# Performance work log

Measured on AMD Instinct MI355X. Metric: run time of the kernel, lower is better.

## Reference

```python
import jax, jax.numpy as jnp
import numpy as np

B, T, D = 4, 4096, 1024
EPS = 1e-5


def _layernorm(x, w):
    mu = jnp.mean(x, axis=-1, keepdims=True)
    var = jnp.var(x, axis=-1, keepdims=True)
    return (x - mu) * jax.lax.rsqrt(var + EPS) * w


def setup_inputs() -> dict:
    key = jax.random.key(0)
    k0, k1, k2, k3 = jax.random.split(key, 4)
    x = jax.random.normal(k0, (B, T, D), dtype=jnp.float32)
    lengths = jax.random.randint(k1, (B,), 1, T + 1, dtype=jnp.int32)
    ln1_w = jnp.ones((D,), dtype=jnp.float32)
    ln2_w = jnp.ones((D,), dtype=jnp.float32)
    Wfc = jax.random.normal(k2, (D, 4 * D), dtype=jnp.float32) * 0.02
    Wproj = jax.random.normal(k3, (4 * D, D), dtype=jnp.float32) * 0.02
    return {"x": x, "lengths": lengths, "ln1_w": ln1_w, "ln2_w": ln2_w,
            "Wfc": Wfc, "Wproj": Wproj}


def reference(x, lengths, ln1_w, ln2_w, Wfc, Wproj):
    b, t, d = x.shape
    # valid[b, i] = i < lengths[b]  (non-padded positions)
    valid = (jnp.arange(t)[None, :] < lengths[:, None]).astype(x.dtype)  # (B,T)

    # --- FusedQueryAtt: out[b,i] = h[b,i] + valid_i * sum_{j<=i} valid_j * gelu(h[b,j])
    h = _layernorm(x, ln1_w)
    g = jax.nn.gelu(h, approximate=False) * valid[:, :, None]  # (B,T,D)
    attn_out = h + valid[:, :, None] * jnp.cumsum(g, axis=1)
    x = x + attn_out  # residual around attn

    # --- MLP (bias=False, dropout=0 in eval)
    h2 = _layernorm(x, ln2_w)
    mlp_out = jax.nn.gelu(h2 @ Wfc, approximate=False) @ Wproj
    return x + mlp_out
```

## Files before the change

### kernel.cpp

```cpp
#include <hip/hip_runtime.h>
#include <hip/hip_bf16.h>
#include <math.h>

#define B_SZ 4
#define T_SZ 4096
#define D_SZ 1024
#define H_SZ 4096
#define CHUNK 16
#define NCHUNK (T_SZ / CHUNK)
#define LN_EPS 1e-5f

using frag8 = __attribute__((ext_vector_type(8))) short;
using f32x4 = __attribute__((ext_vector_type(4))) float;

__device__ __forceinline__ float gelu_exact(float x) {
  return 0.5f * x * (1.0f + erff(x * 0.70710678118654752f));
}

__device__ __forceinline__ float gelu_fast(float x) {
  float u2 = 1.5957691216057308f * (x + 0.044715f * x * x * x);
  float e = __expf(u2);
  return x - x * __builtin_amdgcn_rcpf(e + 1.0f);
}

__device__ __forceinline__ unsigned short f2bf(float f) {
  unsigned u = __float_as_uint(f);
  u += 0x7fffu + ((u >> 16) & 1u);
  return (unsigned short)(u >> 16);
}

__global__ __launch_bounds__(256) void ln_stats(
    const float* __restrict__ x, float2* __restrict__ stats) {
  __shared__ float red[8];
  int tid = threadIdx.x;
  size_t row = (size_t)blockIdx.x * D_SZ;
  float4 v = ((const float4*)(x + row))[tid];
  float s = v.x + v.y + v.z + v.w;
  float q = v.x * v.x + v.y * v.y + v.z * v.z + v.w * v.w;
#pragma unroll
  for (int o = 32; o > 0; o >>= 1) {
    s += __shfl_xor(s, o, 64);
    q += __shfl_xor(q, o, 64);
  }
  int w = tid >> 6;
  if ((tid & 63) == 0) { red[w * 2] = s; red[w * 2 + 1] = q; }
  __syncthreads();
  if (tid == 0) {
    s = red[0] + red[2] + red[4] + red[6];
    q = red[1] + red[3] + red[5] + red[7];
    float mu = s * (1.0f / D_SZ);
    float var = q * (1.0f / D_SZ) - mu * mu;
    float2 st; st.x = mu; st.y = rsqrtf(var + LN_EPS);
    stats[blockIdx.x] = st;
  }
}

__global__ __launch_bounds__(256) void attn_phase1(
    const float* __restrict__ x, const float2* __restrict__ stats,
    const int* __restrict__ lengths, const float* __restrict__ w1,
    float* __restrict__ partial, float* __restrict__ csum) {
  int b = blockIdx.x >> 8;
  int c = blockIdx.x & (NCHUNK - 1);
  int tid = threadIdx.x;
  int len = lengths[b];
  float4 w = ((const float4*)w1)[tid];
  float run0 = 0.f, run1 = 0.f, run2 = 0.f, run3 = 0.f;
#pragma unroll 4
  for (int i = 0; i < CHUNK; ++i) {
    int t = c * CHUNK + i;
    size_t row = ((size_t)b * T_SZ + t) * D_SZ;
    float4 v = ((const float4*)(x + row))[tid];
    float2 st = stats[b * T_SZ + t];
    bool valid = t < len;
    float hx = (v.x - st.x) * st.y * w.x, hy = (v.y - st.x) * st.y * w.y;
    float hz = (v.z - st.x) * st.y * w.z, hw = (v.w - st.x) * st.y * w.w;
    if (valid) {
      run0 += gelu_exact(hx); run1 += gelu_exact(hy);
      run2 += gelu_exact(hz); run3 += gelu_exact(hw);
    }
    float4 p;
    p.x = v.x + hx + (valid ? run0 : 0.f);
    p.y = v.y + hy + (valid ? run1 : 0.f);
    p.z = v.z + hz + (valid ? run2 : 0.f);
    p.w = v.w + hw + (valid ? run3 : 0.f);
    ((float4*)(partial + row))[tid] = p;
  }
  float4 cs; cs.x = run0; cs.y = run1; cs.z = run2; cs.w = run3;
  ((float4*)(csum + ((size_t)b * NCHUNK + c) * D_SZ))[tid] = cs;
}

__global__ __launch_bounds__(256) void chunk_scan(float* __restrict__ csum) {
  int idx = blockIdx.x * 256 + threadIdx.x;
  int b = idx >> 10;
  int d = idx & (D_SZ - 1);
  float* p = csum + (size_t)b * NCHUNK * D_SZ + d;
  float acc = 0.f;
#pragma unroll 8
  for (int c = 0; c < NCHUNK; ++c) {
    float t = p[(size_t)c * D_SZ];
    p[(size_t)c * D_SZ] = acc;
    acc += t;
  }
}

__global__ __launch_bounds__(256) void attn_phase2_ln2(
    float* __restrict__ xres, const float* __restrict__ csum,
    const int* __restrict__ lengths, const float* __restrict__ w2,
    unsigned short* __restrict__ h2) {
  __shared__ float red[8];
  int t = blockIdx.x & (T_SZ - 1);
  int b = blockIdx.x >> 12;
  int tid = threadIdx.x;
  bool valid = t < lengths[b];
  int c = t / CHUNK;
  size_t row = ((size_t)b * T_SZ + t) * D_SZ;
  float4 v = ((const float4*)(xres + row))[tid];
  if (valid) {
    float4 o = ((const float4*)(csum + ((size_t)b * NCHUNK + c) * D_SZ))[tid];
    v.x += o.x; v.y += o.y; v.z += o.z; v.w += o.w;
  }
  ((float4*)(xres + row))[tid] = v;
  float s = v.x + v.y + v.z + v.w;
  float q = v.x * v.x + v.y * v.y + v.z * v.z + v.w * v.w;
#pragma unroll
  for (int o = 32; o > 0; o >>= 1) {
    s += __shfl_xor(s, o, 64);
    q += __shfl_xor(q, o, 64);
  }
  int wv = tid >> 6;
  if ((tid & 63) == 0) { red[wv * 2] = s; red[wv * 2 + 1] = q; }
  __syncthreads();
  s = red[0] + red[2] + red[4] + red[6];
  q = red[1] + red[3] + red[5] + red[7];
  float mu = s * (1.0f / D_SZ);
  float var = q * (1.0f / D_SZ) - mu * mu;
  float rstd = rsqrtf(var + LN_EPS);
  float4 w = ((const float4*)w2)[tid];
  ushort4 hq;
  hq.x = f2bf((v.x - mu) * rstd * w.x);
  hq.y = f2bf((v.y - mu) * rstd * w.y);
  hq.z = f2bf((v.z - mu) * rstd * w.z);
  hq.w = f2bf((v.w - mu) * rstd * w.w);
  ((ushort4*)(h2 + row))[tid] = hq;
}

__global__ __launch_bounds__(256) void transpose_f32_to_bf16(
    const float* __restrict__ src, unsigned short* __restrict__ dst,
    int R, int C) {
  __shared__ float tile[32][33];
  int bx = blockIdx.x * 32;
  int by = blockIdx.y * 32;
  int tx = threadIdx.x & 31;
  int ty = threadIdx.x >> 5;
#pragma unroll
  for (int i = 0; i < 32; i += 8)
    tile[ty + i][tx] = src[(size_t)(by + ty + i) * C + bx + tx];
  __syncthreads();
#pragma unroll
  for (int i = 0; i < 32; i += 8)
    dst[(size_t)(bx + ty + i) * R + by + tx] = f2bf(tile[tx][ty + i]);
}

__device__ __forceinline__ void gld_lds16(const unsigned short* g,
                                          unsigned short* l) {
  __builtin_amdgcn_global_load_lds(
      (const __attribute__((address_space(1))) unsigned int*)g,
      (__attribute__((address_space(3))) unsigned int*)l, 16, 0, 0);
}

#define GT_TILE (256 * 64)

__device__ __forceinline__ void stageA(const unsigned short* A_blk, int K,
                                       unsigned short* as_buf, int h, int k0,
                                       int tid) {
#pragma unroll
  for (int j = 0; j < 2; ++j) {
    int R = j * 128 + h * 64 + (tid >> 3);
    int kc = ((tid & 7) * 8) ^ ((R & 7) << 3);
    gld_lds16(A_blk + (size_t)R * K + k0 + kc,
              as_buf + R * 64 + (tid & 7) * 8);
  }
}

__device__ __forceinline__ void stageB(const unsigned short* B_blk, int K,
                                       unsigned short* bs_buf, int h, int k0,
                                       int tid) {
  int lr = tid >> 3;
#pragma unroll
  for (int j = 0; j < 2; ++j) {
    int R = j * 128 + (lr >> 5) * 64 + h * 32 + (lr & 31);
    int kc = ((tid & 7) * 8) ^ ((R & 7) << 3);
    gld_lds16(B_blk + (size_t)R * K + k0 + kc,
              bs_buf + R * 64 + (tid & 7) * 8);
  }
}

__device__ __forceinline__ void load_afrag(const unsigned short* base,
                                           frag8 (&dst)[4][2], int mh, int wm,
                                           int r16, int quad) {
#pragma unroll
  for (int tm = 0; tm < 4; ++tm)
#pragma unroll
    for (int kk = 0; kk < 2; ++kk) {
      int r = wm * 128 + mh * 64 + tm * 16 + r16;
      int cb = (kk * 64 + quad * 16) ^ ((r16 & 7) << 4);
      dst[tm][kk] = *(const frag8*)(base + r * 64 + (cb >> 1));
    }
}

__device__ __forceinline__ void load_bfrag(const unsigned short* base,
                                           frag8 (&dst)[2][2], int nh, int wn,
                                           int r16, int quad) {
#pragma unroll
  for (int tn = 0; tn < 2; ++tn)
#pragma unroll
    for (int kk = 0; kk < 2; ++kk) {
      int r = wn * 64 + nh * 32 + tn * 16 + r16;
      int cb = (kk * 64 + quad * 16) ^ ((r16 & 7) << 4);
      dst[tn][kk] = *(const frag8*)(base + r * 64 + (cb >> 1));
    }
}

template <int MH, int NH>
__device__ __forceinline__ void mfma_q(f32x4 (&acc)[8][4],
                                       const frag8 (&a)[4][2],
                                       const frag8 (&b)[2][2]) {
#pragma unroll
  for (int kk = 0; kk < 2; ++kk)
#pragma unroll
    for (int tm = 0; tm < 4; ++tm)
#pragma unroll
      for (int tn = 0; tn < 2; ++tn)
        acc[MH * 4 + tm][NH * 2 + tn] =
            __builtin_amdgcn_mfma_f32_16x16x32_bf16(
                a[tm][kk], b[tn][kk], acc[MH * 4 + tm][NH * 2 + tn], 0, 0, 0);
}

#define GBAR()                          \
  do {                                  \
    asm volatile("" ::: "memory");      \
    __builtin_amdgcn_s_barrier();       \
    asm volatile("" ::: "memory");      \
  } while (0)

__global__ __launch_bounds__(512, 2) void gemm256_bt(
    const unsigned short* __restrict__ A, const unsigned short* __restrict__ Bt,
    int N, int K, int gx,
    const float* __restrict__ resid, float* __restrict__ outf,
    unsigned short* __restrict__ outb, int epi) {
  extern __shared__ unsigned short smem[];
  unsigned short* As = smem;
  unsigned short* Bs = smem + 2 * GT_TILE;

  int orig = blockIdx.x, nwg = gridDim.x;
  int wg = orig;
  if ((nwg & 7) == 0) wg = (orig & 7) * (nwg >> 3) + (orig >> 3);
  int bx = wg % gx, by = wg / gx;
  int bm = by * 256, bn = bx * 256;

  int tid = threadIdx.x;
  int lane = tid & 63, wave = tid >> 6;
  int wm = wave >> 2, wn = wave & 3;
  int quad = lane >> 4, r16 = lane & 15;

  const unsigned short* A_blk = A + (size_t)bm * K;
  const unsigned short* B_blk = Bt + (size_t)bn * K;
  int nt = K >> 6;

  f32x4 acc[8][4] = {};
  frag8 af[4][2];
  frag8 b0[2][2], b1[2][2];

  stageA(A_blk, K, As, 0, 0, tid);
  stageA(A_blk, K, As, 1, 0, tid);
  stageB(B_blk, K, Bs, 0, 0, tid);
  stageB(B_blk, K, Bs, 1, 0, tid);
  if (nt > 1) {
    stageA(A_blk, K, As + GT_TILE, 0, 64, tid);
    stageB(B_blk, K, Bs + GT_TILE, 0, 64, tid);
    stageB(B_blk, K, Bs + GT_TILE, 1, 64, tid);
    asm volatile("s_waitcnt vmcnt(6)" ::: "memory");
  } else {
    asm volatile("s_waitcnt vmcnt(0)" ::: "memory");
  }
  GBAR();
  load_bfrag(Bs, b0, 0, wn, r16, quad);

  for (int t = 0; t < nt; ++t) {
    unsigned short* As_c = As + (t & 1) * GT_TILE;
    unsigned short* Bs_c = Bs + (t & 1) * GT_TILE;
    unsigned short* As_n = As + ((t + 1) & 1) * GT_TILE;
    unsigned short* Bs_n = Bs + ((t + 1) & 1) * GT_TILE;
    bool p1 = (t + 1 < nt), p2 = (t + 2 < nt);

    load_afrag(As_c, af, 0, wm, r16, quad);
    if (p1) stageA(A_blk, K, As_n, 1, (t + 1) * 64, tid);
    GBAR();
    __builtin_amdgcn_s_setprio(1);
    mfma_q<0, 0>(acc, af, b0);
    __builtin_amdgcn_s_setprio(0);
    GBAR();

    load_bfrag(Bs_c, b1, 1, wn, r16, quad);
    if (p2) stageA(A_blk, K, As_c, 0, (t + 2) * 64, tid);
    GBAR();
    __builtin_amdgcn_s_setprio(1);
    mfma_q<0, 1>(acc, af, b1);
    __builtin_amdgcn_s_setprio(0);
    GBAR();

    load_afrag(As_c, af, 1, wm, r16, quad);
    if (p2) stageB(B_blk, K, Bs_c, 0, (t + 2) * 64, tid);
    GBAR();
    __builtin_amdgcn_s_setprio(1);
    mfma_q<1, 1>(acc, af, b1);
    __builtin_amdgcn_s_setprio(0);
    GBAR();

    if (p2) {
      stageB(B_blk, K, Bs_c, 1, (t + 2) * 64, tid);
      asm volatile("s_waitcnt vmcnt(6)" ::: "memory");
    } else {
      asm volatile("s_waitcnt vmcnt(0)" ::: "memory");
    }
    GBAR();
    __builtin_amdgcn_s_setprio(1);
    mfma_q<1, 0>(acc, af, b0);
    __builtin_amdgcn_s_setprio(0);
    if (p1) load_bfrag(Bs_n, b0, 0, wn, r16, quad);
    GBAR();
  }

  if (epi == 0) {
#pragma unroll
    for (int mf = 0; mf < 8; ++mf) {
#pragma unroll
      for (int nf = 0; nf < 4; ++nf) {
        int gm0 = bm + wm * 128 + mf * 16 + quad * 4;
        int gn = bn + wn * 64 + nf * 16 + r16;
#pragma unroll
        for (int r = 0; r < 4; ++r)
          outb[(size_t)(gm0 + r) * N + gn] = f2bf(gelu_fast(acc[mf][nf][r]));
      }
    }
  } else {
#pragma unroll
    for (int mf = 0; mf < 8; ++mf) {
#pragma unroll
      for (int nf = 0; nf < 4; ++nf) {
        int gm0 = bm + wm * 128 + mf * 16 + quad * 4;
        int gn = bn + wn * 64 + nf * 16 + r16;
#pragma unroll
        for (int r = 0; r < 4; ++r)
          outf[(size_t)(gm0 + r) * N + gn] =
              resid[(size_t)(gm0 + r) * N + gn] + acc[mf][nf][r];
      }
    }
  }
}

extern "C" void kernel_launch(void* const* d_in, const int* in_sizes, int n_in,
                              void* d_out, int out_size, void* d_ws,
                              size_t ws_size, hipStream_t stream) {
  const float* x = (const float*)d_in[0];
  const int* lengths = (const int*)d_in[1];
  const float* ln1_w = (const float*)d_in[2];
  const float* ln2_w = (const float*)d_in[3];
  const float* Wfc = (const float*)d_in[4];
  const float* Wproj = (const float*)d_in[5];
  float* out = (float*)d_out;

  static bool lds_cfg = false;
  if (!lds_cfg) {
    hipFuncSetAttribute((const void*)gemm256_bt,
                        hipFuncAttributeMaxDynamicSharedMemorySize, 131072);
    lds_cfg = true;
  }

  char* ws = (char*)d_ws;
  size_t off = 0;
  float2* stats = (float2*)(ws + off);
  off += (size_t)B_SZ * T_SZ * sizeof(float2);
  float* csum = (float*)(ws + off);
  off += (size_t)B_SZ * NCHUNK * D_SZ * sizeof(float);
  unsigned short* wfcb = (unsigned short*)(ws + off);
  off += (size_t)D_SZ * H_SZ * sizeof(unsigned short);
  unsigned short* wprojb = (unsigned short*)(ws + off);
  off += (size_t)H_SZ * D_SZ * sizeof(unsigned short);
  unsigned short* h2 = (unsigned short*)(ws + off);
  off += (size_t)B_SZ * T_SZ * D_SZ * sizeof(unsigned short);
  unsigned short* act = (unsigned short*)(ws + off);

  const int M = B_SZ * T_SZ;
  const size_t tileBytes = 256ull * H_SZ * sizeof(unsigned short);
  size_t avail = (ws_size > off) ? (ws_size - off) : 0;
  int sliceTiles = (int)(avail / tileBytes);
  if (sliceTiles < 1) sliceTiles = 1;
  int sliceM = sliceTiles * 256;
  if (sliceM > M) sliceM = M;

  ln_stats<<<B_SZ * T_SZ, 256, 0, stream>>>(x, stats);
  attn_phase1<<<B_SZ * NCHUNK, 256, 0, stream>>>(x, stats, lengths, ln1_w,
                                                 out, csum);
  chunk_scan<<<(B_SZ * D_SZ) / 256, 256, 0, stream>>>(csum);
  attn_phase2_ln2<<<B_SZ * T_SZ, 256, 0, stream>>>(out, csum, lengths, ln2_w, h2);
  transpose_f32_to_bf16<<<dim3(H_SZ / 32, D_SZ / 32), 256, 0, stream>>>(
      Wfc, wfcb, D_SZ, H_SZ);
  transpose_f32_to_bf16<<<dim3(D_SZ / 32, H_SZ / 32), 256, 0, stream>>>(
      Wproj, wprojb, H_SZ, D_SZ);

  for (int m0 = 0; m0 < M; m0 += sliceM) {
    int rows = (M - m0 < sliceM) ? (M - m0) : sliceM;
    int r1 = rows / 256;
    gemm256_bt<<<dim3((H_SZ / 256) * r1), 512, 131072, stream>>>(
        h2 + (size_t)m0 * D_SZ, wfcb, H_SZ, D_SZ, H_SZ / 256,
        nullptr, nullptr, act, 0);
    gemm256_bt<<<dim3((D_SZ / 256) * r1), 512, 131072, stream>>>(
        act, wprojb, D_SZ, H_SZ, D_SZ / 256,
        out + (size_t)m0 * D_SZ, out + (size_t)m0 * D_SZ, nullptr, 1);
  }
}
```

Before: 487.6 us.

## Fuse LN1 stats into phase1, split chunk scan into segments, precompute GEMM addresses

Row mean/variance for the first layernorm are now computed inside attn_phase1, so the separate ln_stats kernel and its extra read of x go away. The single serial chunk scan (16 blocks) becomes a two-level segmented scan over 8 segments, which launches more blocks. The GEMM main loop is unrolled by two, with the double-buffer offsets baked in as compile-time constants and the global and LDS addresses precomputed once, to cut per-iteration address arithmetic. The cost is two block barriers per row inside phase1 and one more kernel launch.

```diff
diff --git a/kernel.cpp b/kernel.cpp
--- a/kernel.cpp
+++ b/kernel.cpp
@@ -8,6 +8,8 @@
 #define H_SZ 4096
 #define CHUNK 16
 #define NCHUNK (T_SZ / CHUNK)
+#define NSEG 8
+#define SEGC (NCHUNK / NSEG)
 #define LN_EPS 1e-5f
 
 using frag8 = __attribute__((ext_vector_type(8))) short;
@@ -29,51 +31,39 @@
   return (unsigned short)(u >> 16);
 }
 
-__global__ __launch_bounds__(256) void ln_stats(
-    const float* __restrict__ x, float2* __restrict__ stats) {
+__global__ __launch_bounds__(256) void attn_phase1(
+    const float* __restrict__ x, const int* __restrict__ lengths,
+    const float* __restrict__ w1, float* __restrict__ partial,
+    float* __restrict__ csum) {
   __shared__ float red[8];
-  int tid = threadIdx.x;
-  size_t row = (size_t)blockIdx.x * D_SZ;
-  float4 v = ((const float4*)(x + row))[tid];
-  float s = v.x + v.y + v.z + v.w;
-  float q = v.x * v.x + v.y * v.y + v.z * v.z + v.w * v.w;
-#pragma unroll
-  for (int o = 32; o > 0; o >>= 1) {
-    s += __shfl_xor(s, o, 64);
-    q += __shfl_xor(q, o, 64);
-  }
-  int w = tid >> 6;
-  if ((tid & 63) == 0) { red[w * 2] = s; red[w * 2 + 1] = q; }
-  __syncthreads();
-  if (tid == 0) {
-    s = red[0] + red[2] + red[4] + red[6];
-    q = red[1] + red[3] + red[5] + red[7];
-    float mu = s * (1.0f / D_SZ);
-    float var = q * (1.0f / D_SZ) - mu * mu;
-    float2 st; st.x = mu; st.y = rsqrtf(var + LN_EPS);
-    stats[blockIdx.x] = st;
-  }
-}
-
-__global__ __launch_bounds__(256) void attn_phase1(
-    const float* __restrict__ x, const float2* __restrict__ stats,
-    const int* __restrict__ lengths, const float* __restrict__ w1,
-    float* __restrict__ partial, float* __restrict__ csum) {
   int b = blockIdx.x >> 8;
   int c = blockIdx.x & (NCHUNK - 1);
   int tid = threadIdx.x;
   int len = lengths[b];
   float4 w = ((const float4*)w1)[tid];
   float run0 = 0.f, run1 = 0.f, run2 = 0.f, run3 = 0.f;
-#pragma unroll 4
   for (int i = 0; i < CHUNK; ++i) {
     int t = c * CHUNK + i;
     size_t row = ((size_t)b * T_SZ + t) * D_SZ;
     float4 v = ((const float4*)(x + row))[tid];
-    float2 st = stats[b * T_SZ + t];
+    float s = v.x + v.y + v.z + v.w;
+    float q = v.x * v.x + v.y * v.y + v.z * v.z + v.w * v.w;
+#pragma unroll
+    for (int o = 32; o > 0; o >>= 1) {
+      s += __shfl_xor(s, o, 64);
+      q += __shfl_xor(q, o, 64);
+    }
+    if ((tid & 63) == 0) { red[(tid >> 6) * 2] = s; red[(tid >> 6) * 2 + 1] = q; }
+    __syncthreads();
+    s = red[0] + red[2] + red[4] + red[6];
+    q = red[1] + red[3] + red[5] + red[7];
+    __syncthreads();
+    float mu = s * (1.0f / D_SZ);
+    float var = q * (1.0f / D_SZ) - mu * mu;
+    float rstd = rsqrtf(var + LN_EPS);
     bool valid = t < len;
-    float hx = (v.x - st.x) * st.y * w.x, hy = (v.y - st.x) * st.y * w.y;
-    float hz = (v.z - st.x) * st.y * w.z, hw = (v.w - st.x) * st.y * w.w;
+    float hx = (v.x - mu) * rstd * w.x, hy = (v.y - mu) * rstd * w.y;
+    float hz = (v.z - mu) * rstd * w.z, hw = (v.w - mu) * rstd * w.w;
     if (valid) {
       run0 += gelu_exact(hx); run1 += gelu_exact(hy);
       run2 += gelu_exact(hz); run3 += gelu_exact(hw);
@@ -89,18 +79,36 @@
   ((float4*)(csum + ((size_t)b * NCHUNK + c) * D_SZ))[tid] = cs;
 }
 
-__global__ __launch_bounds__(256) void chunk_scan(float* __restrict__ csum) {
-  int idx = blockIdx.x * 256 + threadIdx.x;
-  int b = idx >> 10;
-  int d = idx & (D_SZ - 1);
-  float* p = csum + (size_t)b * NCHUNK * D_SZ + d;
+__global__ __launch_bounds__(256) void seg_scan(float* __restrict__ csum,
+                                                float* __restrict__ segsum) {
+  int blk = blockIdx.x;
+  int b = blk >> 5, seg = (blk >> 2) & 7, dq = blk & 3;
+  int d = dq * 256 + threadIdx.x;
+  float* p = csum + ((size_t)b * NCHUNK + seg * SEGC) * D_SZ + d;
   float acc = 0.f;
 #pragma unroll 8
-  for (int c = 0; c < NCHUNK; ++c) {
-    float t = p[(size_t)c * D_SZ];
-    p[(size_t)c * D_SZ] = acc;
-    acc += t;
-  }
+  for (int j = 0; j < SEGC; ++j) {
+    float v = p[(size_t)j * D_SZ];
+    p[(size_t)j * D_SZ] = acc;
+    acc += v;
+  }
+  segsum[((size_t)b * NSEG + seg) * D_SZ + d] = acc;
+}
+
+__global__ __launch_bounds__(256) void seg_apply(
+    float* __restrict__ csum, const float* __restrict__ segsum) {
+  int blk = blockIdx.x;
+  int b = blk >> 5, seg = (blk >> 2) & 7, dq = blk & 3;
+  if (seg == 0) return;
+  int d = dq * 256 + threadIdx.x;
+  float off = 0.f;
+  for (int s = 0; s < NSEG; ++s) {
+    float v = segsum[((size_t)b * NSEG + s) * D_SZ + d];
+    if (s < seg) off += v;
+  }
+  float* p = csum + ((size_t)b * NCHUNK + seg * SEGC) * D_SZ + d;
+#pragma unroll 8
+  for (int j = 0; j < SEGC; ++j) p[(size_t)j * D_SZ] += off;
 }
 
 __global__ __launch_bounds__(256) void attn_phase2_ln2(
@@ -161,64 +169,48 @@
     dst[(size_t)(bx + ty + i) * R + by + tx] = f2bf(tile[tx][ty + i]);
 }
 
-__device__ __forceinline__ void gld_lds16(const unsigned short* g,
-                                          unsigned short* l) {
-  __builtin_amdgcn_global_load_lds(
-      (const __attribute__((address_space(1))) unsigned int*)g,
-      (__attribute__((address_space(3))) unsigned int*)l, 16, 0, 0);
-}
-
 #define GT_TILE (256 * 64)
 
-__device__ __forceinline__ void stageA(const unsigned short* A_blk, int K,
-                                       unsigned short* as_buf, int h, int k0,
-                                       int tid) {
-#pragma unroll
-  for (int j = 0; j < 2; ++j) {
-    int R = j * 128 + h * 64 + (tid >> 3);
-    int kc = ((tid & 7) * 8) ^ ((R & 7) << 3);
-    gld_lds16(A_blk + (size_t)R * K + k0 + kc,
-              as_buf + R * 64 + (tid & 7) * 8);
-  }
-}
-
-__device__ __forceinline__ void stageB(const unsigned short* B_blk, int K,
-                                       unsigned short* bs_buf, int h, int k0,
-                                       int tid) {
-  int lr = tid >> 3;
-#pragma unroll
-  for (int j = 0; j < 2; ++j) {
-    int R = j * 128 + (lr >> 5) * 64 + h * 32 + (lr & 31);
-    int kc = ((tid & 7) * 8) ^ ((R & 7) << 3);
-    gld_lds16(B_blk + (size_t)R * K + k0 + kc,
-              bs_buf + R * 64 + (tid & 7) * 8);
-  }
-}
-
-__device__ __forceinline__ void load_afrag(const unsigned short* base,
-                                           frag8 (&dst)[4][2], int mh, int wm,
-                                           int r16, int quad) {
-#pragma unroll
-  for (int tm = 0; tm < 4; ++tm)
-#pragma unroll
-    for (int kk = 0; kk < 2; ++kk) {
-      int r = wm * 128 + mh * 64 + tm * 16 + r16;
-      int cb = (kk * 64 + quad * 16) ^ ((r16 & 7) << 4);
-      dst[tm][kk] = *(const frag8*)(base + r * 64 + (cb >> 1));
-    }
-}
-
-__device__ __forceinline__ void load_bfrag(const unsigned short* base,
-                                           frag8 (&dst)[2][2], int nh, int wn,
-                                           int r16, int quad) {
-#pragma unroll
-  for (int tn = 0; tn < 2; ++tn)
-#pragma unroll
-    for (int kk = 0; kk < 2; ++kk) {
-      int r = wn * 64 + nh * 32 + tn * 16 + r16;
-      int cb = (kk * 64 + quad * 16) ^ ((r16 & 7) << 4);
-      dst[tn][kk] = *(const frag8*)(base + r * 64 + (cb >> 1));
-    }
+#define GLD16(gsrc, ldsoff)                                                   \
+  __builtin_amdgcn_global_load_lds(                                           \
+      (const __attribute__((address_space(1))) unsigned int*)(gsrc),          \
+      (__attribute__((address_space(3))) unsigned int*)(smc + (ldsoff)), 16,  \
+      0, 0)
+
+#define STAGE_A(h, DP, k0e)                                                   \
+  do {                                                                        \
+    GLD16(gA + (size_t)((h) * 64) * K + (k0e),                                \
+          aW + (h) * 8192 + (DP) * 32768);                                    \
+    GLD16(gA + (size_t)((h) * 64 + 128) * K + (k0e),                          \
+          aW + (h) * 8192 + 16384 + (DP) * 32768);                            \
+  } while (0)
+
+#define STAGE_B(h, DP, k0e)                                                   \
+  do {                                                                        \
+    GLD16(gB + (size_t)((h) * 32) * K + (k0e),                                \
+          bW + (h) * 4096 + (DP) * 32768);                                    \
+    GLD16(gB + (size_t)((h) * 32 + 128) * K + (k0e),                          \
+          bW + (h) * 4096 + 16384 + (DP) * 32768);                            \
+  } while (0)
+
+template <int CUR, int MH>
+__device__ __forceinline__ void rd_af(const char* smc, int aB0, int aB1,
+                                      frag8 (&af)[4][2]) {
+#pragma unroll
+  for (int tm = 0; tm < 4; ++tm) {
+    af[tm][0] = *(const frag8*)(smc + aB0 + (CUR + MH * 8192 + tm * 2048));
+    af[tm][1] = *(const frag8*)(smc + aB1 + (CUR + MH * 8192 + tm * 2048));
+  }
+}
+
+template <int CUR, int NH>
+__device__ __forceinline__ void rd_bf(const char* smc, int bB0, int bB1,
+                                      frag8 (&bf)[2][2]) {
+#pragma unroll
+  for (int tn = 0; tn < 2; ++tn) {
+    bf[tn][0] = *(const frag8*)(smc + bB0 + (CUR + NH * 4096 + tn * 2048));
+    bf[tn][1] = *(const frag8*)(smc + bB1 + (CUR + NH * 4096 + tn * 2048));
+  }
 }
 
 template <int MH, int NH>
@@ -243,14 +235,54 @@
     asm volatile("" ::: "memory");      \
   } while (0)
 
+#define TILE_BODY(t, CURB, CURP, NXTB, NXTP)                                  \
+  do {                                                                        \
+    bool p1 = (t) + 1 < nt, p2 = (t) + 2 < nt;                                \
+                     \
+    rd_af<CURB, 0>(smc, aB0, aB1, af);                                        \
+    if (p1) STAGE_A(1, NXTP, ((t) + 1) * 64);                                 \
+    GBAR();                                                                   \
+    __builtin_amdgcn_s_setprio(1);                                            \
+    mfma_q<0, 0>(acc, af, b0);                                                \
+    __builtin_amdgcn_s_setprio(0);                                            \
+    GBAR();                                                                   \
+           \
+    rd_bf<CURB, 1>(smc, bB0, bB1, b1);                                        \
+    if (p2) STAGE_A(0, CURP, ((t) + 2) * 64);                                 \
+    GBAR();                                                                   \
+    __builtin_amdgcn_s_setprio(1);                                            \
+    mfma_q<0, 1>(acc, af, b1);                                                \
+    __builtin_amdgcn_s_setprio(0);                                            \
+    GBAR();                                                                   \
+      \
+    rd_af<CURB, 1>(smc, aB0, aB1, af);                                        \
+    if (p2) STAGE_B(0, CURP, ((t) + 2) * 64);                                 \
+    GBAR();                                                                   \
+    __builtin_amdgcn_s_setprio(1);                                            \
+    mfma_q<1, 1>(acc, af, b1);                                                \
+    __builtin_amdgcn_s_setprio(0);                                            \
+    GBAR();                                                                   \
+                 \
+    if (p2) {                                                                 \
+      STAGE_B(1, CURP, ((t) + 2) * 64);                                       \
+      asm volatile("s_waitcnt vmcnt(6)" ::: "memory");                        \
+    } else {                                                                  \
+      asm volatile("s_waitcnt vmcnt(0)" ::: "memory");                        \
+    }                                                                         \
+    GBAR();                                                                   \
+    __builtin_amdgcn_s_setprio(1);                                            \
+    mfma_q<1, 0>(acc, af, b0);                                                \
+    __builtin_amdgcn_s_setprio(0);                                            \
+    if (p1) rd_bf<NXTB, 0>(smc, bB0, bB1, b0);                                \
+    GBAR();                                                                   \
+  } while (0)
+
 __global__ __launch_bounds__(512, 2) void gemm256_bt(
     const unsigned short* __restrict__ A, const unsigned short* __restrict__ Bt,
     int N, int K, int gx,
     const float* __restrict__ resid, float* __restrict__ outf,
     unsigned short* __restrict__ outb, int epi) {
-  extern __shared__ unsigned short smem[];
-  unsigned short* As = smem;
-  unsigned short* Bs = smem + 2 * GT_TILE;
+  extern __shared__ char smc[];
 
   int orig = blockIdx.x, nwg = gridDim.x;
   int wg = orig;
@@ -267,68 +299,42 @@
   const unsigned short* B_blk = Bt + (size_t)bn * K;
   int nt = K >> 6;
 
+  int swz = (r16 & 7) << 4;
+  int aB0 = wm * 16384 + r16 * 128 + ((quad * 16) ^ swz);
+  int aB1 = wm * 16384 + r16 * 128 + ((64 + quad * 16) ^ swz);
+  int bB0 = 65536 + wn * 8192 + r16 * 128 + ((quad * 16) ^ swz);
+  int bB1 = 65536 + wn * 8192 + r16 * 128 + ((64 + quad * 16) ^ swz);
+
+  int arow = tid >> 3;
+  int kc = ((tid & 7) * 8) ^ ((arow & 7) << 3);
+  const unsigned short* gA = A_blk + (size_t)arow * K + kc;
+  int browl = (arow >> 5) * 64 + (arow & 31);
+  const unsigned short* gB = B_blk + (size_t)browl * K + kc;
+  int aW = arow * 128 + (tid & 7) * 16;
+  int bW = 65536 + browl * 128 + (tid & 7) * 16;
+
   f32x4 acc[8][4] = {};
   frag8 af[4][2];
   frag8 b0[2][2], b1[2][2];
 
-  stageA(A_blk, K, As, 0, 0, tid);
-  stageA(A_blk, K, As, 1, 0, tid);
-  stageB(B_blk, K, Bs, 0, 0, tid);
-  stageB(B_blk, K, Bs, 1, 0, tid);
+  STAGE_A(0, 0, 0);
+  STAGE_A(1, 0, 0);
+  STAGE_B(0, 0, 0);
+  STAGE_B(1, 0, 0);
   if (nt > 1) {
-    stageA(A_blk, K, As + GT_TILE, 0, 64, tid);
-    stageB(B_blk, K, Bs + GT_TILE, 0, 64, tid);
-    stageB(B_blk, K, Bs + GT_TILE, 1, 64, tid);
+    STAGE_A(0, 1, 64);
+    STAGE_B(0, 1, 64);
+    STAGE_B(1, 1, 64);
     asm volatile("s_waitcnt vmcnt(6)" ::: "memory");
   } else {
     asm volatile("s_waitcnt vmcnt(0)" ::: "memory");
   }
   GBAR();
-  load_bfrag(Bs, b0, 0, wn, r16, quad);
-
-  for (int t = 0; t < nt; ++t) {
-    unsigned short* As_c = As + (t & 1) * GT_TILE;
-    unsigned short* Bs_c = Bs + (t & 1) * GT_TILE;
-    unsigned short* As_n = As + ((t + 1) & 1) * GT_TILE;
-    unsigned short* Bs_n = Bs + ((t + 1) & 1) * GT_TILE;
-    bool p1 = (t + 1 < nt), p2 = (t + 2 < nt);
-
-    load_afrag(As_c, af, 0, wm, r16, quad);
-    if (p1) stageA(A_blk, K, As_n, 1, (t + 1) * 64, tid);
-    GBAR();
-    __builtin_amdgcn_s_setprio(1);
-    mfma_q<0, 0>(acc, af, b0);
-    __builtin_amdgcn_s_setprio(0);
-    GBAR();
-
-    load_bfrag(Bs_c, b1, 1, wn, r16, quad);
-    if (p2) stageA(A_blk, K, As_c, 0, (t + 2) * 64, tid);
-    GBAR();
-    __builtin_amdgcn_s_setprio(1);
-    mfma_q<0, 1>(acc, af, b1);
-    __builtin_amdgcn_s_setprio(0);
-    GBAR();
-
-    load_afrag(As_c, af, 1, wm, r16, quad);
-    if (p2) stageB(B_blk, K, Bs_c, 0, (t + 2) * 64, tid);
-    GBAR();
-    __builtin_amdgcn_s_setprio(1);
-    mfma_q<1, 1>(acc, af, b1);
-    __builtin_amdgcn_s_setprio(0);
-    GBAR();
-
-    if (p2) {
-      stageB(B_blk, K, Bs_c, 1, (t + 2) * 64, tid);
-      asm volatile("s_waitcnt vmcnt(6)" ::: "memory");
-    } else {
-      asm volatile("s_waitcnt vmcnt(0)" ::: "memory");
-    }
-    GBAR();
-    __builtin_amdgcn_s_setprio(1);
-    mfma_q<1, 0>(acc, af, b0);
-    __builtin_amdgcn_s_setprio(0);
-    if (p1) load_bfrag(Bs_n, b0, 0, wn, r16, quad);
-    GBAR();
+  rd_bf<0, 0>(smc, bB0, bB1, b0);
+
+  for (int t = 0; t < nt; t += 2) {
+    TILE_BODY(t, 0, 0, 32768, 1);
+    TILE_BODY(t + 1, 32768, 1, 0, 0);
   }
 
   if (epi == 0) {
@@ -379,8 +385,8 @@
 
   char* ws = (char*)d_ws;
   size_t off = 0;
-  float2* stats = (float2*)(ws + off);
-  off += (size_t)B_SZ * T_SZ * sizeof(float2);
+  float* segsum = (float*)(ws + off);
+  off += (size_t)B_SZ * NSEG * D_SZ * sizeof(float);
   float* csum = (float*)(ws + off);
   off += (size_t)B_SZ * NCHUNK * D_SZ * sizeof(float);
   unsigned short* wfcb = (unsigned short*)(ws + off);
@@ -399,10 +405,9 @@
   int sliceM = sliceTiles * 256;
   if (sliceM > M) sliceM = M;
 
-  ln_stats<<<B_SZ * T_SZ, 256, 0, stream>>>(x, stats);
-  attn_phase1<<<B_SZ * NCHUNK, 256, 0, stream>>>(x, stats, lengths, ln1_w,
-                                                 out, csum);
-  chunk_scan<<<(B_SZ * D_SZ) / 256, 256, 0, stream>>>(csum);
+  attn_phase1<<<B_SZ * NCHUNK, 256, 0, stream>>>(x, lengths, ln1_w, out, csum);
+  seg_scan<<<B_SZ * NSEG * (D_SZ / 256), 256, 0, stream>>>(csum, segsum);
+  seg_apply<<<B_SZ * NSEG * (D_SZ / 256), 256, 0, stream>>>(csum, segsum);
   attn_phase2_ln2<<<B_SZ * T_SZ, 256, 0, stream>>>(out, csum, lengths, ln2_w, h2);
   transpose_f32_to_bf16<<<dim3(H_SZ / 32, D_SZ / 32), 256, 0, stream>>>(
       Wfc, wfcb, D_SZ, H_SZ);
```

New measurement: 458.4 us. 1.06x faster.
